# Kernel optimization log

Hardware: AMD Instinct MI355X
Metric: run time of the kernel (lower is better)

The kernel has to match this reference:

```python
import jax, jax.numpy as jnp
import numpy as np
import math

B, N, K, H = 2, 2048, 1024, 16
S = K // H  # head dim = 64


def apply_rope(t):
    # t: [b, h, N, s] -> rotary position embedding (rotate-half convention)
    s = t.shape[-1]
    pos = jnp.arange(t.shape[2], dtype=jnp.float32)
    inv_freq = 1.0 / (10000.0 ** (jnp.arange(0, s, 2, dtype=jnp.float32) / s))
    ang = pos[:, None] * inv_freq[None, :]               # [N, s/2]
    cos = jnp.concatenate([jnp.cos(ang), jnp.cos(ang)], axis=-1)  # [N, s]
    sin = jnp.concatenate([jnp.sin(ang), jnp.sin(ang)], axis=-1)
    t1, t2 = t[..., : s // 2], t[..., s // 2:]
    rot = jnp.concatenate([-t2, t1], axis=-1)
    return t * cos + rot * sin


def setup_inputs() -> dict:
    key = jax.random.key(0)
    ks = jax.random.split(key, 6)
    sc = 1.0 / math.sqrt(K)
    x = jax.random.normal(ks[0], (B, N, K), dtype=jnp.float32)
    Wq = jax.random.normal(ks[1], (K, K), dtype=jnp.float32) * sc
    Wk = jax.random.normal(ks[2], (K, K), dtype=jnp.float32) * sc
    Wv = jax.random.normal(ks[3], (K, K), dtype=jnp.float32) * sc
    Wu = jax.random.normal(ks[4], (K, K), dtype=jnp.float32) * sc
    bu = jax.random.normal(ks[5], (K,), dtype=jnp.float32) * 0.01
    mask = jnp.tril(jnp.ones((N, N), dtype=jnp.int32))  # causal
    return {"x": x, "Wq": Wq, "Wk": Wk, "Wv": Wv, "Wu": Wu, "bu": bu, "mask": mask}


def reference(x, Wq, Wk, Wv, Wu, bu, mask):
    b, n, k = x.shape
    h, s = H, S
    # torch Linear: y = x @ W.T
    def proj(W):
        return (x @ W.T).reshape(b, n, h, s).transpose(0, 2, 1, 3)  # [b,h,n,s]
    Q = apply_rope(proj(Wq))
    Kh = apply_rope(proj(Wk))
    V = proj(Wv)
    scores = jnp.einsum('bhqs,bhks->bhqk', Q, Kh) / math.sqrt(s)
    scores = jnp.where(mask[None, None, :, :] == 0, -jnp.inf, scores)
    attn = jax.nn.softmax(scores, axis=-1)
    out = jnp.einsum('bhqk,bhks->bhqs', attn, V)           # [b,h,n,s]
    out = out.transpose(0, 2, 1, 3).reshape(b, n, k)
    return out @ Wu.T + bu
```

## Files before the change

kernel.cpp:

```cpp
#include <hip/hip_runtime.h>
#include <hip/hip_bf16.h>

#define Bq 2
#define Nq 2048
#define Kq 1024
#define Hq 16
#define Sq 64
#define Mq (Bq * Nq)

typedef __attribute__((ext_vector_type(4))) float f32x4;
typedef __attribute__((ext_vector_type(8))) short bf16x8;

__device__ unsigned short g_xb[(size_t)Mq * Kq];
__device__ unsigned short g_Wqb[Kq * Kq];
__device__ unsigned short g_Wkb[Kq * Kq];
__device__ unsigned short g_Wvb[Kq * Kq];
__device__ unsigned short g_Wub[Kq * Kq];
__device__ unsigned short g_Qb[(size_t)Bq * Hq * Nq * Sq];
__device__ unsigned short g_Kb[(size_t)Bq * Hq * Nq * Sq];
__device__ unsigned short g_Vt[(size_t)Bq * Hq * Sq * Nq];
__device__ unsigned short g_Ao[(size_t)Mq * Kq];
__device__ __align__(16) float g_On[(size_t)32 * 16 * 3 * 128 * 64];
__device__ float g_Ol[32 * 16 * 3 * 128];

__constant__ signed char c_qt[30] = {15,15,15,14,14,14,13,13,13,12,12,12,11,11,10,10,9,9,8,8,7,7,6,6,5,4,3,2,1,0};
__constant__ signed char c_t0[30] = {0,11,22,0,10,20,0,10,19,0,9,18,0,12,0,11,0,10,0,9,0,8,0,7,0,0,0,0,0,0};
__constant__ signed char c_t1[30] = {11,22,32,10,20,30,10,19,28,9,18,26,12,24,11,22,10,20,9,18,8,16,7,14,12,10,8,6,4,2};
__constant__ signed char c_sp[30] = {0,1,2,0,1,2,0,1,2,0,1,2,0,1,0,1,0,1,0,1,0,1,0,1,0,0,0,0,0,0};
__constant__ signed char c_ns[30] = {3,3,3,3,3,3,3,3,3,3,3,3,2,2,2,2,2,2,2,2,2,2,2,2,1,1,1,1,1,1};

__device__ __forceinline__ unsigned short f2bf(float f) {
    union { float f; unsigned int i; } u; u.f = f;
    unsigned int r = u.i + 0x7FFF + ((u.i >> 16) & 1);
    return (unsigned short)(r >> 16);
}
__device__ __forceinline__ float bf2f(unsigned short u) {
    union { unsigned int i; float f; } v; v.i = ((unsigned int)u) << 16;
    return v.f;
}
__device__ __forceinline__ void async16(const unsigned short* g, unsigned short* l) {
    __builtin_amdgcn_global_load_lds(
        (const __attribute__((address_space(1))) void*)g,
        (__attribute__((address_space(3))) void*)l, 16, 0, 0);
}

__global__ __launch_bounds__(256) void convert_all_kernel(
    const float* __restrict__ x,  const float* __restrict__ wq,
    const float* __restrict__ wk, const float* __restrict__ wv,
    const float* __restrict__ wu)
{
    int i = blockIdx.x * 256 + threadIdx.x;
    const float* src; unsigned short* dst; int off;
    if (i < 1048576) { src = x; dst = g_xb; off = i; }
    else {
        int j = i - 1048576;
        int which = j >> 18;
        off = j & 262143;
        src = (which == 0) ? wq : (which == 1) ? wk : (which == 2) ? wv : wu;
        dst = (which == 0) ? g_Wqb : (which == 1) ? g_Wkb : (which == 2) ? g_Wvb : g_Wub;
    }
    float4 v = ((const float4*)src)[off];
    ushort4 o;
    o.x = f2bf(v.x); o.y = f2bf(v.y); o.z = f2bf(v.z); o.w = f2bf(v.w);
    ((ushort4*)dst)[off] = o;
}

__global__ __launch_bounds__(512, 2) void qkv_gemm_kernel()
{
    __shared__ __align__(16) unsigned short SLDS[65536];
    auto As = (unsigned short (*)[256][64])(SLDS);
    auto Bs = (unsigned short (*)[256][64])(SLDS + 32768);

    const int n0 = blockIdx.x * 256;
    const int m0 = blockIdx.y * 256;
    const int which = n0 >> 10;
    const unsigned short* A  = g_xb;
    const unsigned short* Bm = (which == 0) ? g_Wqb : (which == 1) ? g_Wkb : g_Wvb;
    const int nb = n0 & 1023;

    const int tid = threadIdx.x;
    const int w = tid >> 6, l = tid & 63;
    const int lane16 = l & 15, quad = l >> 4;
    const int wr = w >> 2, wc = w & 3;
    const int sr8 = l >> 3;
    const int sc  = ((l & 7) ^ sr8) * 8;
    const int rsw = lane16 & 7;

    f32x4 acc[8][4];
#pragma unroll
    for (int mf = 0; mf < 8; ++mf)
#pragma unroll
        for (int nf = 0; nf < 4; ++nf) acc[mf][nf] = (f32x4){0.f, 0.f, 0.f, 0.f};

#define STG_A(t, b, c) async16(A  + (size_t)(m0 + (c)*64 + w*8 + sr8) * Kq + (t)*64 + sc, \
                               &As[(b)][(c)*64 + w*8][0])
#define STG_B(t, b, c) async16(Bm + (size_t)(nb + (c)*64 + w*8 + sr8) * Kq + (t)*64 + sc, \
                               &Bs[(b)][(c)*64 + w*8][0])

    STG_B(0, 0, 0); STG_B(0, 0, 1); STG_B(0, 0, 2); STG_B(0, 0, 3);
    STG_A(0, 0, 0); STG_A(0, 0, 2); STG_A(0, 0, 1); STG_A(0, 0, 3);
    asm volatile("s_waitcnt vmcnt(2)" ::: "memory");
    __builtin_amdgcn_s_barrier();

    int cur = 0;
    for (int t = 0; t < 16; ++t) {
        const bool stg = (t + 1 < 16);
        const int nxt = cur ^ 1;
        bf16x8 bf[4][2];
#pragma unroll
        for (int q = 0; q < 4; ++q) {
            asm volatile("" ::: "memory");
            bf16x8 af[2][2];
            if (q == 0) {
#pragma unroll
                for (int nf = 0; nf < 4; ++nf)
#pragma unroll
                    for (int ks = 0; ks < 2; ++ks)
                        bf[nf][ks] = *(const bf16x8*)
                            &Bs[cur][wc * 64 + nf * 16 + lane16][((ks * 4 + quad) ^ rsw) * 8];
            }
#pragma unroll
            for (int m2 = 0; m2 < 2; ++m2)
#pragma unroll
                for (int ks = 0; ks < 2; ++ks)
                    af[m2][ks] = *(const bf16x8*)
                        &As[cur][wr * 128 + (q * 2 + m2) * 16 + lane16][((ks * 4 + quad) ^ rsw) * 8];
            if (stg) {
                if (q == 0) { STG_B(t + 1, nxt, 0); STG_B(t + 1, nxt, 1); }
                if (q == 1) { STG_B(t + 1, nxt, 2); STG_B(t + 1, nxt, 3); }
                if (q == 2) { STG_A(t + 1, nxt, 0); STG_A(t + 1, nxt, 2); }
                if (q == 3) { STG_A(t + 1, nxt, 1); STG_A(t + 1, nxt, 3); }
            }
            asm volatile("" ::: "memory");
            __builtin_amdgcn_s_barrier();
            asm volatile("s_waitcnt lgkmcnt(0)" ::: "memory");
            __builtin_amdgcn_sched_barrier(0);
            __builtin_amdgcn_s_setprio(1);
#pragma unroll
            for (int m2 = 0; m2 < 2; ++m2)
#pragma unroll
                for (int nf = 0; nf < 4; ++nf)
#pragma unroll
                    for (int ks = 0; ks < 2; ++ks)
                        acc[q * 2 + m2][nf] = __builtin_amdgcn_mfma_f32_16x16x32_bf16(
                            af[m2][ks], bf[nf][ks], acc[q * 2 + m2][nf], 0, 0, 0);
            __builtin_amdgcn_s_setprio(0);
            if (q == 1) {
                if (stg) asm volatile("s_waitcnt vmcnt(4)" ::: "memory");
                else     asm volatile("s_waitcnt vmcnt(0)" ::: "memory");
            }
            if (q == 3) {
                if (stg) asm volatile("s_waitcnt vmcnt(2)" ::: "memory");
                else     asm volatile("s_waitcnt vmcnt(0)" ::: "memory");
            }
            __builtin_amdgcn_s_barrier();
        }
        cur ^= 1;
    }
#undef STG_A
#undef STG_B

    const int h0q = nb >> 6;
    if (which < 2) {
        unsigned short* dst = (which == 0) ? g_Qb : g_Kb;
        const int h = h0q + wc;
        const float invf0 = exp2f((float)lane16 * -0.41524101f);
        const float invf1 = exp2f((float)(lane16 + 16) * -0.41524101f);
#pragma unroll
        for (int mf = 0; mf < 8; ++mf)
#pragma unroll
            for (int r = 0; r < 4; ++r) {
                int m = m0 + wr * 128 + mf * 16 + quad * 4 + r;
                int b = m >> 11, nn = m & 2047;
                float np = (float)nn;
                float a0 = np * invf0, a1 = np * invf1;
                float s0 = __sinf(a0), c0 = __cosf(a0);
                float s1 = __sinf(a1), c1 = __cosf(a1);
                float t10 = acc[mf][0][r], t20 = acc[mf][2][r];
                float t11 = acc[mf][1][r], t21 = acc[mf][3][r];
                unsigned short* dr = dst + (((size_t)b * Hq + h) * Nq + nn) * Sq + lane16;
                dr[0]  = f2bf(t10 * c0 - t20 * s0);
                dr[16] = f2bf(t11 * c1 - t21 * s1);
                dr[32] = f2bf(t20 * c0 + t10 * s0);
                dr[48] = f2bf(t21 * c1 + t11 * s1);
            }
    } else {
        unsigned short* T = SLDS;
        const int b = m0 >> 11, mcol = m0 & 2047;
#pragma unroll
        for (int pass = 0; pass < 2; ++pass) {
            __syncthreads();
            if (wr == pass) {
#pragma unroll
                for (int mf = 0; mf < 8; ++mf)
#pragma unroll
                    for (int nf = 0; nf < 4; ++nf)
#pragma unroll
                        for (int r = 0; r < 4; ++r)
                            T[(wc * 64 + nf * 16 + lane16) * 136 + mf * 16 + quad * 4 + r] =
                                f2bf(acc[mf][nf][r]);
            }
            __syncthreads();
            {
                int row = tid >> 1;
                int h = h0q + (row >> 6), s = row & 63;
                unsigned short* drow = g_Vt + (((size_t)b * Hq + h) * Sq + s) * Nq
                                        + mcol + pass * 128 + (tid & 1) * 64;
                const unsigned short* srow = T + row * 136 + (tid & 1) * 64;
#pragma unroll
                for (int jj = 0; jj < 8; ++jj)
                    *(uint4*)(drow + jj * 8) = *(const uint4*)(srow + jj * 8);
            }
        }
    }
}

__global__ __launch_bounds__(512) void attn_kernel()
{
    const int bh = blockIdx.x;
    const int y  = blockIdx.y;
    const int qt  = c_qt[y];
    const int t0  = c_t0[y];
    const int t1  = c_t1[y];
    const int sp  = c_sp[y];
    const int nsp = c_ns[y];
    const int q0 = qt * 128;
    const unsigned short* Qp = g_Qb + (size_t)bh * Nq * Sq;
    const unsigned short* Kp = g_Kb + (size_t)bh * Nq * Sq;
    const unsigned short* Vp = g_Vt + (size_t)bh * Sq * Nq;

    __shared__ __align__(16) unsigned short Ks[3][64][64];
    __shared__ __align__(16) unsigned short Vs[3][64][64];
    __shared__ __align__(16) unsigned short Ps[128][64];
    unsigned short* psf = &Ps[0][0];

    const int tid = threadIdx.x;
    const int w = tid >> 6, l = tid & 63;
    const int lane16 = l & 15, quad = l >> 4;
    const int sr = l >> 3;
    const int sc = ((l & 7) ^ sr) * 8;
    const int rsw = (lane16 & 7);

    bf16x8 be;
    {
        short o = (lane16 == 0) ? (short)0x3F80 : (short)0;
#pragma unroll
        for (int i = 0; i < 8; ++i) be[i] = o;
    }

    const int qlo = q0 + 16 * w;
    bf16x8 aq0 = *(const bf16x8*)(Qp + (size_t)(qlo + lane16) * Sq + quad * 8);
    bf16x8 aq1 = *(const bf16x8*)(Qp + (size_t)(qlo + lane16) * Sq + quad * 8 + 32);
    asm volatile("" : "+v"(aq0), "+v"(aq1));

    f32x4 Oacc[4];
    f32x4 Oext = (f32x4){0.f, 0.f, 0.f, 0.f};
#pragma unroll
    for (int ds = 0; ds < 4; ++ds) Oacc[ds] = (f32x4){0.f, 0.f, 0.f, 0.f};

    const float C1 = 0.18033688f;
    const float C2 = 11.54156036f;

#define STAGE(t, b)                                                           \
    do {                                                                      \
        int kn_ = (t) * 64;                                                   \
        async16(Kp + (size_t)(kn_ + 8 * w + sr) * Sq + sc, &Ks[(b)][8 * w][0]);\
        async16(Vp + (size_t)(8 * w + sr) * Nq + kn_ + sc, &Vs[(b)][8 * w][0]);\
    } while (0)

    STAGE(t0, 0);
    STAGE(t0 + 1, 1);
    asm volatile("s_waitcnt vmcnt(2)" ::: "memory");
    __builtin_amdgcn_s_barrier();
    __builtin_amdgcn_sched_barrier(0);

    int cur = 0;
    for (int kb = t0; kb < t1; ++kb) {
        if (kb + 2 < t1) STAGE(kb + 2, (kb - t0 + 2) % 3);

        if (kb * 64 <= qlo + 15) {
            f32x4 S[4];
#pragma unroll
            for (int kc = 0; kc < 4; ++kc) S[kc] = (f32x4){0.f, 0.f, 0.f, 0.f};
#pragma unroll
            for (int kc = 0; kc < 4; ++kc) {
                const unsigned short* krow = &Ks[cur][kc * 16 + lane16][0];
                bf16x8 bk0 = *(const bf16x8*)&krow[(quad ^ rsw) * 8];
                bf16x8 bk1 = *(const bf16x8*)&krow[((4 + quad) ^ rsw) * 8];
                S[kc] = __builtin_amdgcn_mfma_f32_16x16x32_bf16(aq0, bk0, S[kc], 0, 0, 0);
                S[kc] = __builtin_amdgcn_mfma_f32_16x16x32_bf16(aq1, bk1, S[kc], 0, 0, 0);
            }

            const int qbase = qlo + quad * 4;
            if (kb * 64 + 63 > qlo) {
#pragma unroll
                for (int kc = 0; kc < 4; ++kc) {
                    int kpos = kb * 64 + kc * 16 + lane16;
#pragma unroll
                    for (int r = 0; r < 4; ++r)
                        S[kc][r] = (kpos <= qbase + r) ? exp2f(fmaf(S[kc][r], C1, -C2)) : 0.0f;
                }
            } else {
#pragma unroll
                for (int kc = 0; kc < 4; ++kc)
#pragma unroll
                    for (int r = 0; r < 4; ++r)
                        S[kc][r] = exp2f(fmaf(S[kc][r], C1, -C2));
            }

#pragma unroll
            for (int kc = 0; kc < 4; ++kc)
#pragma unroll
                for (int r = 0; r < 4; ++r) {
                    int prow = 16 * w + quad * 4 + r;
                    psf[(prow * 64 + kc * 16 + lane16) ^ ((prow & 7) << 3)] =
                        (unsigned short)(__float_as_uint(S[kc][r]) >> 16);
                }

            const int prow2 = 16 * w + lane16;
#pragma unroll
            for (int kk = 0; kk < 2; ++kk) {
                bf16x8 pa = *(const bf16x8*)(psf +
                    ((prow2 * 64 + kk * 32 + quad * 8) ^ (rsw << 3)));
#pragma unroll
                for (int ds = 0; ds < 4; ++ds) {
                    bf16x8 vb = *(const bf16x8*)&Vs[cur][ds * 16 + lane16][((kk * 4 + quad) ^ rsw) * 8];
                    Oacc[ds] = __builtin_amdgcn_mfma_f32_16x16x32_bf16(pa, vb, Oacc[ds], 0, 0, 0);
                }
                Oext = __builtin_amdgcn_mfma_f32_16x16x32_bf16(pa, be, Oext, 0, 0, 0);
            }
        }

        __builtin_amdgcn_sched_barrier(0);
        if (kb + 2 < t1) {
            asm volatile("s_waitcnt vmcnt(2)" ::: "memory");
        } else {
            asm volatile("s_waitcnt vmcnt(0)" ::: "memory");
        }
        __builtin_amdgcn_s_barrier();
        __builtin_amdgcn_sched_barrier(0);
        cur = (cur == 2) ? 0 : cur + 1;
    }
#undef STAGE

    if (nsp == 1) {
        const int b = bh >> 4, h = bh & 15;
        float inv[4];
#pragma unroll
        for (int r = 0; r < 4; ++r) {
            float lr = __shfl(Oext[r], quad * 16, 64);
            inv[r] = 1.0f / lr;
        }
#pragma unroll
        for (int ds = 0; ds < 4; ++ds)
#pragma unroll
            for (int r = 0; r < 4; ++r) {
                int nn = qlo + quad * 4 + r;
                g_Ao[((size_t)b * Nq + nn) * Kq + h * Sq + ds * 16 + lane16] =
                    f2bf(Oacc[ds][r] * inv[r]);
            }
    } else {
        float* On = g_On + (((size_t)bh * 16 + qt) * 3 + sp) * (128 * 64);
        float* Ol = g_Ol + (((size_t)bh * 16 + qt) * 3 + sp) * 128;
#pragma unroll
        for (int r = 0; r < 4; ++r) {
            float lr = __shfl(Oext[r], quad * 16, 64);
            if (lane16 == 0) Ol[16 * w + quad * 4 + r] = lr;
        }
#pragma unroll
        for (int ds = 0; ds < 4; ++ds)
#pragma unroll
            for (int r = 0; r < 4; ++r)
                On[(16 * w + quad * 4 + r) * 64 + ds * 16 + lane16] = Oacc[ds][r];
    }
}

__global__ __launch_bounds__(256) void attn_combine_kernel()
{
    const int bh = blockIdx.x;
    const int qt = 6 + blockIdx.y;
    const int nsp = (qt >= 12) ? 3 : 2;
    const int tid = threadIdx.x;
    const int row = tid >> 1;
    const int ch  = (tid & 1) * 32;
    const size_t sb = ((size_t)bh * 16 + qt) * 3;
    const float* On0 = g_On + (sb + 0) * (128 * 64);
    const float* On1 = g_On + (sb + 1) * (128 * 64);
    const float* On2 = g_On + (sb + 2) * (128 * 64);
    const float* Ol  = g_Ol + sb * 128;

    float lsum = Ol[row] + Ol[128 + row];
    if (nsp == 3) lsum += Ol[256 + row];
    float inv = 1.0f / lsum;

    const int b = bh >> 4, h = bh & 15, nn = qt * 128 + row;
    unsigned short* dst = g_Ao + ((size_t)b * Nq + nn) * Kq + h * Sq + ch;

#pragma unroll
    for (int j = 0; j < 8; ++j) {
        int o = row * 64 + ch + j * 4;
        f32x4 v = *(const f32x4*)(On0 + o);
        v += *(const f32x4*)(On1 + o);
        if (nsp == 3) v += *(const f32x4*)(On2 + o);
        ushort4 u;
        u.x = f2bf(v[0] * inv); u.y = f2bf(v[1] * inv);
        u.z = f2bf(v[2] * inv); u.w = f2bf(v[3] * inv);
        ((ushort4*)dst)[j] = u;
    }
}

__global__ __launch_bounds__(256) void out_gemm_kernel(
    const float* __restrict__ bu, float* __restrict__ out)
{
    __shared__ __align__(16) unsigned short As[2][128][64];
    __shared__ __align__(16) unsigned short Bs[2][128][64];

    const int n0 = blockIdx.x * 128;
    const int m0 = blockIdx.y * 128;

    const int tid = threadIdx.x;
    const int w = tid >> 6, l = tid & 63;
    const int lane16 = l & 15, quad = l >> 4;
    const int wm = (w >> 1) * 64, wn = (w & 1) * 64;
    const int sr = l >> 3;
    const int sc = ((l & 7) ^ sr) * 8;
    const int rsw = (lane16 & 7);

    f32x4 acc[4][4];
#pragma unroll
    for (int mi = 0; mi < 4; ++mi)
#pragma unroll
        for (int ni = 0; ni < 4; ++ni) acc[mi][ni] = (f32x4){0.f, 0.f, 0.f, 0.f};

#pragma unroll
    for (int c = 0; c < 4; ++c) {
        async16(g_Ao  + (size_t)(m0 + 32 * w + 8 * c + sr) * Kq + sc, &As[0][32 * w + 8 * c][0]);
        async16(g_Wub + (size_t)(n0 + 32 * w + 8 * c + sr) * Kq + sc, &Bs[0][32 * w + 8 * c][0]);
    }
    __syncthreads();

    int cur = 0;
    for (int kt = 0; kt < Kq; kt += 64) {
        if (kt + 64 < Kq) {
            int nxt = cur ^ 1;
#pragma unroll
            for (int c = 0; c < 4; ++c) {
                async16(g_Ao  + (size_t)(m0 + 32 * w + 8 * c + sr) * Kq + kt + 64 + sc, &As[nxt][32 * w + 8 * c][0]);
                async16(g_Wub + (size_t)(n0 + 32 * w + 8 * c + sr) * Kq + kt + 64 + sc, &Bs[nxt][32 * w + 8 * c][0]);
            }
        }
#pragma unroll
        for (int ks = 0; ks < 2; ++ks) {
            bf16x8 af[4], bfr[4];
#pragma unroll
            for (int mi = 0; mi < 4; ++mi)
                af[mi]  = *(const bf16x8*)&As[cur][wm + mi * 16 + lane16][((ks * 4 + quad) ^ rsw) * 8];
#pragma unroll
            for (int ni = 0; ni < 4; ++ni)
                bfr[ni] = *(const bf16x8*)&Bs[cur][wn + ni * 16 + lane16][((ks * 4 + quad) ^ rsw) * 8];
#pragma unroll
            for (int mi = 0; mi < 4; ++mi)
#pragma unroll
                for (int ni = 0; ni < 4; ++ni)
                    acc[mi][ni] = __builtin_amdgcn_mfma_f32_16x16x32_bf16(af[mi], bfr[ni], acc[mi][ni], 0, 0, 0);
        }
        __syncthreads();
        cur ^= 1;
    }

#pragma unroll
    for (int mi = 0; mi < 4; ++mi)
#pragma unroll
        for (int ni = 0; ni < 4; ++ni)
#pragma unroll
            for (int r = 0; r < 4; ++r) {
                int m = m0 + wm + mi * 16 + quad * 4 + r;
                int n = n0 + wn + ni * 16 + lane16;
                out[(size_t)m * Kq + n] = acc[mi][ni][r] + bu[n];
            }
}

extern "C" void kernel_launch(void* const* d_in, const int* in_sizes, int n_in,
                              void* d_out, int out_size, void* d_ws, size_t ws_size,
                              hipStream_t stream)
{
    const float* x  = (const float*)d_in[0];
    const float* Wq = (const float*)d_in[1];
    const float* Wk = (const float*)d_in[2];
    const float* Wv = (const float*)d_in[3];
    const float* Wu = (const float*)d_in[4];
    const float* bu = (const float*)d_in[5];
    float* out = (float*)d_out;

    convert_all_kernel<<<8192, 256, 0, stream>>>(x, Wq, Wk, Wv, Wu);
    qkv_gemm_kernel<<<dim3(12, 16), 512, 0, stream>>>();
    attn_kernel<<<dim3(32, 30), 512, 0, stream>>>();
    attn_combine_kernel<<<dim3(32, 10), 256, 0, stream>>>();
    out_gemm_kernel<<<dim3(8, 32), 256, 0, stream>>>(bu, out);
}
```

Baseline: 215.8 us.

## Fuse split-KV combine into attention via atomic counter; retile output GEMM

Removes the separate attention-combine launch. The last split block for each (bh, q-tile) is chosen by an atomic ticket after a threadfence, and that block reduces the partial outputs and writes g_Ao. The output projection GEMM is also reworked into 256x128 tiles with 512 threads, staged async loads, manual waitcnt/barrier scheduling and setprio around the MFMA bursts. The intent is to save a launch plus the gap between kernels and to raise GEMM efficiency, but the grid shrinks to 128 blocks on a chip with many CUs, which risks underutilization.

```diff
diff --git a/kernel.cpp b/kernel.cpp
--- a/kernel.cpp
+++ b/kernel.cpp
@@ -22,6 +22,7 @@
 __device__ unsigned short g_Ao[(size_t)Mq * Kq];
 __device__ __align__(16) float g_On[(size_t)32 * 16 * 3 * 128 * 64];
 __device__ float g_Ol[32 * 16 * 3 * 128];
+__device__ int g_cnt[320];
 
 __constant__ signed char c_qt[30] = {15,15,15,14,14,14,13,13,13,12,12,12,11,11,10,10,9,9,8,8,7,7,6,6,5,4,3,2,1,0};
 __constant__ signed char c_t0[30] = {0,11,22,0,10,20,0,10,19,0,9,18,0,12,0,11,0,10,0,9,0,8,0,7,0,0,0,0,0,0};
@@ -49,6 +50,7 @@
     const float* __restrict__ wk, const float* __restrict__ wv,
     const float* __restrict__ wu)
 {
+    if (blockIdx.x == 0 && threadIdx.x < 320) g_cnt[threadIdx.x] = 0;
     int i = blockIdx.x * 256 + threadIdx.x;
     const float* src; unsigned short* dst; int off;
     if (i < 1048576) { src = x; dst = g_xb; off = i; }
@@ -232,6 +234,7 @@
     __shared__ __align__(16) unsigned short Ks[3][64][64];
     __shared__ __align__(16) unsigned short Vs[3][64][64];
     __shared__ __align__(16) unsigned short Ps[128][64];
+    __shared__ int s_tk;
     unsigned short* psf = &Ps[0][0];
 
     const int tid = threadIdx.x;
@@ -372,111 +375,137 @@
 #pragma unroll
             for (int r = 0; r < 4; ++r)
                 On[(16 * w + quad * 4 + r) * 64 + ds * 16 + lane16] = Oacc[ds][r];
-    }
-}
-
-__global__ __launch_bounds__(256) void attn_combine_kernel()
-{
-    const int bh = blockIdx.x;
-    const int qt = 6 + blockIdx.y;
-    const int nsp = (qt >= 12) ? 3 : 2;
-    const int tid = threadIdx.x;
-    const int row = tid >> 1;
-    const int ch  = (tid & 1) * 32;
-    const size_t sb = ((size_t)bh * 16 + qt) * 3;
-    const float* On0 = g_On + (sb + 0) * (128 * 64);
-    const float* On1 = g_On + (sb + 1) * (128 * 64);
-    const float* On2 = g_On + (sb + 2) * (128 * 64);
-    const float* Ol  = g_Ol + sb * 128;
-
-    float lsum = Ol[row] + Ol[128 + row];
-    if (nsp == 3) lsum += Ol[256 + row];
-    float inv = 1.0f / lsum;
-
-    const int b = bh >> 4, h = bh & 15, nn = qt * 128 + row;
-    unsigned short* dst = g_Ao + ((size_t)b * Nq + nn) * Kq + h * Sq + ch;
-
-#pragma unroll
-    for (int j = 0; j < 8; ++j) {
-        int o = row * 64 + ch + j * 4;
-        f32x4 v = *(const f32x4*)(On0 + o);
-        v += *(const f32x4*)(On1 + o);
-        if (nsp == 3) v += *(const f32x4*)(On2 + o);
-        ushort4 u;
-        u.x = f2bf(v[0] * inv); u.y = f2bf(v[1] * inv);
-        u.z = f2bf(v[2] * inv); u.w = f2bf(v[3] * inv);
-        ((ushort4*)dst)[j] = u;
-    }
-}
-
-__global__ __launch_bounds__(256) void out_gemm_kernel(
+
+        __threadfence();
+        __syncthreads();
+        if (tid == 0) s_tk = atomicAdd(&g_cnt[bh * 10 + (qt - 6)], 1);
+        __syncthreads();
+        if (s_tk == nsp - 1) {
+            const float* On0 = g_On + (((size_t)bh * 16 + qt) * 3) * (128 * 64);
+            const float* Ol0 = g_Ol + (((size_t)bh * 16 + qt) * 3) * 128;
+            const int row = tid >> 2;
+            const int c0  = (tid & 3) * 16;
+            float ls = Ol0[row] + Ol0[128 + row];
+            if (nsp == 3) ls += Ol0[256 + row];
+            float inv = 1.0f / ls;
+            const int b = bh >> 4, h = bh & 15, nn = q0 + row;
+            unsigned short* dstp = g_Ao + ((size_t)b * Nq + nn) * Kq + h * Sq + c0;
+#pragma unroll
+            for (int j = 0; j < 4; ++j) {
+                int o = row * 64 + c0 + j * 4;
+                f32x4 v = *(const f32x4*)(On0 + o);
+                v += *(const f32x4*)(On0 + 8192 + o);
+                if (nsp == 3) v += *(const f32x4*)(On0 + 16384 + o);
+                ushort4 u;
+                u.x = f2bf(v[0] * inv); u.y = f2bf(v[1] * inv);
+                u.z = f2bf(v[2] * inv); u.w = f2bf(v[3] * inv);
+                *(ushort4*)(dstp + j * 4) = u;
+            }
+        }
+    }
+}
+
+__global__ __launch_bounds__(512, 1) void out_gemm_kernel(
     const float* __restrict__ bu, float* __restrict__ out)
 {
-    __shared__ __align__(16) unsigned short As[2][128][64];
-    __shared__ __align__(16) unsigned short Bs[2][128][64];
+    __shared__ __align__(16) unsigned short SLDS[49152];
+    auto As = (unsigned short (*)[256][64])(SLDS);
+    auto Bs = (unsigned short (*)[128][64])(SLDS + 32768);
 
     const int n0 = blockIdx.x * 128;
-    const int m0 = blockIdx.y * 128;
+    const int m0 = blockIdx.y * 256;
 
     const int tid = threadIdx.x;
     const int w = tid >> 6, l = tid & 63;
     const int lane16 = l & 15, quad = l >> 4;
-    const int wm = (w >> 1) * 64, wn = (w & 1) * 64;
-    const int sr = l >> 3;
-    const int sc = ((l & 7) ^ sr) * 8;
-    const int rsw = (lane16 & 7);
-
-    f32x4 acc[4][4];
-#pragma unroll
-    for (int mi = 0; mi < 4; ++mi)
-#pragma unroll
-        for (int ni = 0; ni < 4; ++ni) acc[mi][ni] = (f32x4){0.f, 0.f, 0.f, 0.f};
-
-#pragma unroll
-    for (int c = 0; c < 4; ++c) {
-        async16(g_Ao  + (size_t)(m0 + 32 * w + 8 * c + sr) * Kq + sc, &As[0][32 * w + 8 * c][0]);
-        async16(g_Wub + (size_t)(n0 + 32 * w + 8 * c + sr) * Kq + sc, &Bs[0][32 * w + 8 * c][0]);
-    }
-    __syncthreads();
+    const int wr = w >> 2, wc = w & 3;
+    const int sr8 = l >> 3;
+    const int sc  = ((l & 7) ^ sr8) * 8;
+    const int rsw = lane16 & 7;
+
+    f32x4 acc[8][2];
+#pragma unroll
+    for (int mf = 0; mf < 8; ++mf)
+#pragma unroll
+        for (int nf = 0; nf < 2; ++nf) acc[mf][nf] = (f32x4){0.f, 0.f, 0.f, 0.f};
+
+#define OST_A(t, b, c) async16(g_Ao  + (size_t)(m0 + (c)*64 + w*8 + sr8) * Kq + (t)*64 + sc, \
+                               &As[(b)][(c)*64 + w*8][0])
+#define OST_B(t, b, c) async16(g_Wub + (size_t)(n0 + (c)*64 + w*8 + sr8) * Kq + (t)*64 + sc, \
+                               &Bs[(b)][(c)*64 + w*8][0])
+
+    OST_B(0, 0, 0); OST_B(0, 0, 1);
+    OST_A(0, 0, 0); OST_A(0, 0, 2);
+    OST_A(0, 0, 1); OST_A(0, 0, 3);
+    asm volatile("s_waitcnt vmcnt(2)" ::: "memory");
+    __builtin_amdgcn_s_barrier();
 
     int cur = 0;
-    for (int kt = 0; kt < Kq; kt += 64) {
-        if (kt + 64 < Kq) {
-            int nxt = cur ^ 1;
-#pragma unroll
-            for (int c = 0; c < 4; ++c) {
-                async16(g_Ao  + (size_t)(m0 + 32 * w + 8 * c + sr) * Kq + kt + 64 + sc, &As[nxt][32 * w + 8 * c][0]);
-                async16(g_Wub + (size_t)(n0 + 32 * w + 8 * c + sr) * Kq + kt + 64 + sc, &Bs[nxt][32 * w + 8 * c][0]);
-            }
-        }
-#pragma unroll
-        for (int ks = 0; ks < 2; ++ks) {
-            bf16x8 af[4], bfr[4];
-#pragma unroll
-            for (int mi = 0; mi < 4; ++mi)
-                af[mi]  = *(const bf16x8*)&As[cur][wm + mi * 16 + lane16][((ks * 4 + quad) ^ rsw) * 8];
-#pragma unroll
-            for (int ni = 0; ni < 4; ++ni)
-                bfr[ni] = *(const bf16x8*)&Bs[cur][wn + ni * 16 + lane16][((ks * 4 + quad) ^ rsw) * 8];
-#pragma unroll
-            for (int mi = 0; mi < 4; ++mi)
-#pragma unroll
-                for (int ni = 0; ni < 4; ++ni)
-                    acc[mi][ni] = __builtin_amdgcn_mfma_f32_16x16x32_bf16(af[mi], bfr[ni], acc[mi][ni], 0, 0, 0);
-        }
-        __syncthreads();
+    for (int t = 0; t < 16; ++t) {
+        const bool stg = (t + 1 < 16);
+        const int nxt = cur ^ 1;
+        bf16x8 bf[2][2];
+#pragma unroll
+        for (int q = 0; q < 4; ++q) {
+            asm volatile("" ::: "memory");
+            bf16x8 af[2][2];
+            if (q == 0) {
+#pragma unroll
+                for (int nf = 0; nf < 2; ++nf)
+#pragma unroll
+                    for (int ks = 0; ks < 2; ++ks)
+                        bf[nf][ks] = *(const bf16x8*)
+                            &Bs[cur][wc * 32 + nf * 16 + lane16][((ks * 4 + quad) ^ rsw) * 8];
+            }
+#pragma unroll
+            for (int m2 = 0; m2 < 2; ++m2)
+#pragma unroll
+                for (int ks = 0; ks < 2; ++ks)
+                    af[m2][ks] = *(const bf16x8*)
+                        &As[cur][wr * 128 + (q * 2 + m2) * 16 + lane16][((ks * 4 + quad) ^ rsw) * 8];
+            if (stg) {
+                if (q == 0) { OST_B(t + 1, nxt, 0); OST_B(t + 1, nxt, 1); }
+                if (q == 1) { OST_A(t + 1, nxt, 0); OST_A(t + 1, nxt, 2); }
+                if (q == 2) { OST_A(t + 1, nxt, 1); OST_A(t + 1, nxt, 3); }
+            }
+            asm volatile("" ::: "memory");
+            __builtin_amdgcn_s_barrier();
+            asm volatile("s_waitcnt lgkmcnt(0)" ::: "memory");
+            __builtin_amdgcn_sched_barrier(0);
+            __builtin_amdgcn_s_setprio(1);
+#pragma unroll
+            for (int m2 = 0; m2 < 2; ++m2)
+#pragma unroll
+                for (int nf = 0; nf < 2; ++nf)
+#pragma unroll
+                    for (int ks = 0; ks < 2; ++ks)
+                        acc[q * 2 + m2][nf] = __builtin_amdgcn_mfma_f32_16x16x32_bf16(
+                            af[m2][ks], bf[nf][ks], acc[q * 2 + m2][nf], 0, 0, 0);
+            __builtin_amdgcn_s_setprio(0);
+            if (q == 1) {
+                if (stg) asm volatile("s_waitcnt vmcnt(4)" ::: "memory");
+                else     asm volatile("s_waitcnt vmcnt(0)" ::: "memory");
+            }
+            if (q == 3) {
+                if (stg) asm volatile("s_waitcnt vmcnt(2)" ::: "memory");
+                else     asm volatile("s_waitcnt vmcnt(0)" ::: "memory");
+            }
+            __builtin_amdgcn_s_barrier();
+        }
         cur ^= 1;
     }
-
-#pragma unroll
-    for (int mi = 0; mi < 4; ++mi)
-#pragma unroll
-        for (int ni = 0; ni < 4; ++ni)
+#undef OST_A
+#undef OST_B
+
+#pragma unroll
+    for (int mf = 0; mf < 8; ++mf)
+#pragma unroll
+        for (int nf = 0; nf < 2; ++nf)
 #pragma unroll
             for (int r = 0; r < 4; ++r) {
-                int m = m0 + wm + mi * 16 + quad * 4 + r;
-                int n = n0 + wn + ni * 16 + lane16;
-                out[(size_t)m * Kq + n] = acc[mi][ni][r] + bu[n];
+                int m = m0 + wr * 128 + mf * 16 + quad * 4 + r;
+                int n = n0 + wc * 32 + nf * 16 + lane16;
+                out[(size_t)m * Kq + n] = acc[mf][nf][r] + bu[n];
             }
 }
 
@@ -495,6 +524,5 @@
     convert_all_kernel<<<8192, 256, 0, stream>>>(x, Wq, Wk, Wv, Wu);
     qkv_gemm_kernel<<<dim3(12, 16), 512, 0, stream>>>();
     attn_kernel<<<dim3(32, 30), 512, 0, stream>>>();
-    attn_combine_kernel<<<dim3(32, 10), 256, 0, stream>>>();
-    out_gemm_kernel<<<dim3(8, 32), 256, 0, stream>>>(bu, out);
-}
+    out_gemm_kernel<<<dim3(8, 16), 512, 0, stream>>>(bu, out);
+}
```

New measurement: 450.1 us. 2.09x slower.
